# Kernel optimization log

Measured on AMD Instinct MI355X. Metric: run time of the kernel, lower is better.

Reference implementation:

```python
import jax, jax.numpy as jnp
import numpy as np

HEADS = 8
DIM = 512
DIM_HEAD = DIM // 8        # 64
M = DIM // 2               # 256 landmarks
PINV_ITERS = 6
KERNEL = 33                # residual depthwise conv kernel (33,1)


def moore_penrose_pinv(x, iters):
    # x: [b, h, m, m]; Newton-Schulz style iterative pseudoinverse (lucidrains impl)
    abs_x = jnp.abs(x)
    col = abs_x.sum(axis=-1)
    row = abs_x.sum(axis=-2)
    z = jnp.swapaxes(x, -1, -2) / (jnp.max(col) * jnp.max(row))
    I = jnp.eye(x.shape[-1], dtype=x.dtype)
    for _ in range(iters):
        xz = x @ z
        z = 0.25 * z @ (13.0 * I - xz @ (15.0 * I - xz @ (7.0 * I - xz)))
    return z


def setup_inputs() -> dict:
    key = jax.random.key(0)
    ks = jax.random.split(key, 5)
    b, n, dim = 4, 8192, DIM
    x = jax.random.normal(ks[0], (b, n, dim), dtype=jnp.float32)
    # to_qkv: Linear(dim, 3*inner_dim, bias=False); inner_dim = heads*dim_head = dim
    w_qkv = jax.random.normal(ks[1], (dim, 3 * dim), dtype=jnp.float32) / np.sqrt(dim)
    # to_out: Linear(inner_dim, dim) with bias (dropout = identity in eval)
    w_out = jax.random.normal(ks[2], (dim, dim), dtype=jnp.float32) / np.sqrt(dim)
    b_out = jax.random.normal(ks[3], (dim,), dtype=jnp.float32) * 0.01
    # res_conv: Conv2d(heads, heads, (33,1), padding=(16,0), groups=heads, bias=False)
    conv_w = jax.random.normal(ks[4], (HEADS, 1, KERNEL, 1), dtype=jnp.float32) / np.sqrt(KERNEL)
    return {"x": x, "w_qkv": w_qkv, "w_out": w_out, "b_out": b_out, "conv_w": conv_w}


def nystrom_attention(x, w_qkv, w_out, b_out, conv_w):
    b, n, dim = x.shape
    h, d, m = HEADS, DIM_HEAD, M
    # pad front so seq len divisible by num_landmarks (no-op for n=8192, m=256)
    pad = (m - n % m) % m
    xp = jnp.pad(x, ((0, 0), (pad, 0), (0, 0)))
    np_ = n + pad

    qkv = xp @ w_qkv                                   # [b, np, 3*dim]
    q, k, v = jnp.split(qkv, 3, axis=-1)
    to_heads = lambda t: t.reshape(b, np_, h, d).transpose(0, 2, 1, 3)  # [b,h,np,d]
    q, k, v = to_heads(q), to_heads(k), to_heads(v)
    q = q * (d ** -0.5)

    l = np_ // m                                       # tokens per landmark
    pool = lambda t: t.reshape(b, h, m, l, d).mean(axis=3)  # [b,h,m,d]
    q_l, k_l = pool(q), pool(k)

    attn1 = jax.nn.softmax(jnp.einsum('bhnd,bhmd->bhnm', q, k_l), axis=-1)    # [b,h,np,m]
    attn2 = jax.nn.softmax(jnp.einsum('bhid,bhjd->bhij', q_l, k_l), axis=-1)  # [b,h,m,m]
    attn3 = jax.nn.softmax(jnp.einsum('bhmd,bhnd->bhmn', q_l, k), axis=-1)    # [b,h,m,np]

    attn2_inv = moore_penrose_pinv(attn2, PINV_ITERS)
    out = (attn1 @ attn2_inv) @ (attn3 @ v)            # [b,h,np,d]

    # depthwise conv residual over the sequence axis, per head
    res = jax.lax.conv_general_dilated(
        v, conv_w, window_strides=(1, 1),
        padding=((KERNEL // 2, KERNEL // 2), (0, 0)),
        dimension_numbers=('NCHW', 'OIHW', 'NCHW'),
        feature_group_count=h)
    out = out + res

    out = out.transpose(0, 2, 1, 3).reshape(b, np_, dim)
    out = out @ w_out + b_out
    return out[:, -n:]


def reference(x, w_qkv, w_out, b_out, conv_w):
    return x + nystrom_attention(x, w_qkv, w_out, b_out, conv_w)
```

## Files before the change

kernel.cpp:

```cpp
#include <hip/hip_runtime.h>


#define N_SEQ 8192
#define DMODEL 512
#define NHEAD 8
#define DHEAD 64
#define NLAND 256
#define BH 32

typedef unsigned short u16;
typedef __attribute__((ext_vector_type(8))) short bh8;
typedef __attribute__((ext_vector_type(4))) float fx4;

__device__ __forceinline__ float bf2f(u16 u) { return __uint_as_float(((unsigned)u) << 16); }
__device__ __forceinline__ u16 f2bf(float f) {
    unsigned x = __float_as_uint(f);
    return (u16)((x + 0x7fffu + ((x >> 16) & 1u)) >> 16);
}
__device__ __forceinline__ fx4 mfma16(bh8 a, bh8 b, fx4 c) {
    return __builtin_amdgcn_mfma_f32_16x16x32_bf16(a, b, c, 0, 0, 0);
}
__device__ __forceinline__ void gload16(u16* lds, const u16* g) {
    __builtin_amdgcn_global_load_lds(
        (const __attribute__((address_space(1))) unsigned int*)g,
        (__attribute__((address_space(3))) unsigned int*)lds, 16, 0, 0);
}

__global__ void detect_kernel(const u16* __restrict__ X, unsigned* flag_out)
{
    __shared__ int cnt;
    if (threadIdx.x == 0) cnt = 0;
    __syncthreads();
    u16 u = X[threadIdx.x * 2];
    int e = (u >> 7) & 0xFF;
    int insane = (u != 0) && (e < 90 || e > 140);
    atomicAdd(&cnt, insane);
    __syncthreads();
    if (threadIdx.x == 0) flag_out[0] = (cnt > 64) ? 1u : 0u;
}

__global__ __launch_bounds__(256) void convert_kernel(
    const void* __restrict__ in, u16* __restrict__ out, int n, const unsigned* __restrict__ flag)
{
    int i = blockIdx.x * 256 + threadIdx.x;
    if (i >= n) return;
    if (flag[0]) out[i] = f2bf(((const float*)in)[i]);
    else         out[i] = ((const u16*)in)[i];
}

__global__ __launch_bounds__(256) void wtrans_kernel(
    const void* __restrict__ in, u16* __restrict__ out, int rows, int cols,
    const unsigned* __restrict__ flag)
{
    int idx = blockIdx.x * 256 + threadIdx.x;
    if (idx >= rows * cols) return;
    int r = idx / cols, c = idx % cols;
    float v = flag[0] ? ((const float*)in)[idx] : bf2f(((const u16*)in)[idx]);
    out[(size_t)c * rows + r] = f2bf(v);
}

__global__ __launch_bounds__(256) void f2b_kernel(const float* __restrict__ in, u16* __restrict__ out, int n)
{
    int i = blockIdx.x * 256 + threadIdx.x;
    if (i < n) out[i] = f2bf(in[i]);
}

__global__ __launch_bounds__(256) void qkv_mfma_kernel(
    const u16* __restrict__ X, const u16* __restrict__ WT,
    u16* __restrict__ Q, u16* __restrict__ K, u16* __restrict__ VT)
{
    __shared__ u16 Xs[128 * 64];
    __shared__ u16 Ws[128 * 64];
    const int tid = threadIdx.x;
    const int wave = tid >> 6, lane = tid & 63;
    const int wrow = (wave >> 1) * 64, wcol = (wave & 1) * 64;
    const int i0 = blockIdx.x * 128;
    const int j0 = blockIdx.y * 128;
    const int la = lane >> 3, lb = lane & 7;
    const int lm = lane & 15, lq = lane >> 4;
    const int sw = lm & 7;
    const int sc = (lb ^ la) * 8;
    fx4 acc[4][4];
#pragma unroll
    for (int a = 0; a < 4; ++a)
#pragma unroll
        for (int b = 0; b < 4; ++b) acc[a][b] = (fx4){0.f, 0.f, 0.f, 0.f};

    for (int k0 = 0; k0 < DMODEL; k0 += 64) {
        __syncthreads();
#pragma unroll
        for (int jj = 0; jj < 4; ++jj) {
            int rb = wave * 32 + jj * 8;
            gload16(Xs + rb * 64, X + (size_t)(i0 + rb + la) * DMODEL + k0 + sc);
            gload16(Ws + rb * 64, WT + (size_t)(j0 + rb + la) * DMODEL + k0 + sc);
        }
        __syncthreads();
#pragma unroll
        for (int ks = 0; ks < 2; ++ks) {
            const int po = ((ks * 4 + lq) ^ sw) * 8;
            bh8 xf[4], wf[4];
#pragma unroll
            for (int im = 0; im < 4; ++im)
                xf[im] = *(const bh8*)(Xs + (wrow + im * 16 + lm) * 64 + po);
#pragma unroll
            for (int in = 0; in < 4; ++in)
                wf[in] = *(const bh8*)(Ws + (wcol + in * 16 + lm) * 64 + po);
#pragma unroll
            for (int im = 0; im < 4; ++im)
#pragma unroll
                for (int in = 0; in < 4; ++in)
                    acc[im][in] = mfma16(wf[in], xf[im], acc[im][in]);
        }
    }
#pragma unroll
    for (int im = 0; im < 4; ++im) {
        int m = i0 + wrow + im * 16 + lm;
        int bb = m >> 13, ns = m & (N_SEQ - 1);
#pragma unroll
        for (int in = 0; in < 4; ++in) {
            int nn = j0 + wcol + in * 16 + (lq << 2);
            int which = nn >> 9;
            int h = (nn >> 6) & 7;
            int d = nn & 63;
            if (which == 2) {
                size_t vb = (size_t)(bb * NHEAD + h) * DHEAD;
#pragma unroll
                for (int cc = 0; cc < 4; ++cc)
                    VT[(vb + d + cc) * N_SEQ + ns] = f2bf(acc[im][in][cc]);
            } else {
                u16* dst = (which == 0) ? Q : K;
                float s = (which == 0) ? 0.125f : 1.f;
                ushort4 o;
                o.x = f2bf(acc[im][in][0] * s); o.y = f2bf(acc[im][in][1] * s);
                o.z = f2bf(acc[im][in][2] * s); o.w = f2bf(acc[im][in][3] * s);
                *(ushort4*)(dst + ((size_t)(bb * NHEAD + h) * N_SEQ + ns) * DHEAD + d) = o;
            }
        }
    }
}

__global__ __launch_bounds__(64) void pool_kernel(
    const u16* __restrict__ Q, const u16* __restrict__ K,
    float* __restrict__ QL, float* __restrict__ KL,
    u16* __restrict__ QLb, u16* __restrict__ KLb)
{
    int m = blockIdx.x, bh = blockIdx.y, d = threadIdx.x;
    size_t base = ((size_t)bh * N_SEQ + m * 32) * DHEAD + d;
    float sq = 0.f, sk = 0.f;
#pragma unroll
    for (int i = 0; i < 32; ++i) {
        sq += bf2f(Q[base + i * DHEAD]);
        sk += bf2f(K[base + i * DHEAD]);
    }
    size_t ob = ((size_t)bh * NLAND + m) * DHEAD + d;
    sq *= (1.f / 32.f); sk *= (1.f / 32.f);
    QL[ob] = sq; KL[ob] = sk;
    QLb[ob] = f2bf(sq); KLb[ob] = f2bf(sk);
}

__global__ __launch_bounds__(256) void attn2_kernel(
    const float* __restrict__ QL, const float* __restrict__ KL, float* __restrict__ A2)
{
    __shared__ float qrow[64];
    __shared__ float red[256];
    int i = blockIdx.x, bh = blockIdx.y, j = threadIdx.x;
    if (j < 64) qrow[j] = QL[((size_t)bh * NLAND + i) * DHEAD + j];
    __syncthreads();
    const float* kr = KL + ((size_t)bh * NLAND + j) * DHEAD;
    float lg = 0.f;
#pragma unroll
    for (int d = 0; d < 64; ++d) lg += qrow[d] * kr[d];
    red[j] = lg; __syncthreads();
    for (int s = 128; s > 0; s >>= 1) { if (j < s) red[j] = fmaxf(red[j], red[j + s]); __syncthreads(); }
    float mx = red[0]; __syncthreads();
    float p = __expf(lg - mx);
    red[j] = p; __syncthreads();
    for (int s = 128; s > 0; s >>= 1) { if (j < s) red[j] += red[j + s]; __syncthreads(); }
    float sum = red[0];
    A2[((size_t)bh * NLAND + i) * NLAND + j] = p / sum;
}

__global__ void init_scal_kernel(unsigned* scal) { if (threadIdx.x < 2) scal[threadIdx.x] = 0u; }

__global__ __launch_bounds__(256) void absmax_kernel(const float* __restrict__ A2, unsigned* scal)
{
    __shared__ float red[256];
    int bh = blockIdx.x, t = threadIdx.x;
    const float* Ab = A2 + (size_t)bh * 65536;
    float cs = 0.f, rs = 0.f;
    for (int j = 0; j < 256; ++j) cs += fabsf(Ab[t * 256 + j]);
    for (int i = 0; i < 256; ++i) rs += fabsf(Ab[i * 256 + t]);
    red[t] = cs; __syncthreads();
    for (int s = 128; s > 0; s >>= 1) { if (t < s) red[t] = fmaxf(red[t], red[t + s]); __syncthreads(); }
    if (t == 0) atomicMax(scal + 0, __float_as_uint(red[0]));
    __syncthreads();
    red[t] = rs; __syncthreads();
    for (int s = 128; s > 0; s >>= 1) { if (t < s) red[t] = fmaxf(red[t], red[t + s]); __syncthreads(); }
    if (t == 0) atomicMax(scal + 1, __float_as_uint(red[0]));
}

__global__ __launch_bounds__(256) void z0_kernel(
    const float* __restrict__ A2, const unsigned* __restrict__ scal,
    u16* __restrict__ zb, u16* __restrict__ zbT)
{
    float inv = 1.f / (__uint_as_float(scal[0]) * __uint_as_float(scal[1]));
    size_t idx = (size_t)blockIdx.x * 256 + threadIdx.x;
    size_t bh = idx >> 16;
    int r = (int)(idx & 65535);
    int i = r >> 8, j = r & 255;
    zb[idx]  = f2bf(A2[(bh << 16) + (size_t)j * 256 + i] * inv);
    zbT[idx] = f2bf(A2[idx] * inv);
}

__global__ __launch_bounds__(256) void bgemm_mfma_kernel(
    const u16* __restrict__ A, const u16* __restrict__ BT,
    u16* __restrict__ Cn, u16* __restrict__ Ct, const u16* __restrict__ E,
    int N, long sB, long sCn, long sCt, float sc, float alpha, float beta, int wn, int wt)
{
    __shared__ u16 As[64 * 40];
    __shared__ u16 Bs[64 * 40];
    const int tid = threadIdx.x;
    const int wave = tid >> 6, lane = tid & 63;
    const int wm = (wave >> 1) * 32, wnn = (wave & 1) * 32;
    const int i0 = blockIdx.x * 64, j0 = blockIdx.y * 64, bh = blockIdx.z;
    const u16* Ab = A + (size_t)bh * 65536;
    const u16* Bb = BT + (size_t)bh * sB;
    const int lr = tid >> 2, lk = (tid & 3) * 8;
    const int lm = lane & 15, lq = lane >> 4;
    fx4 acc[2][2];
#pragma unroll
    for (int a = 0; a < 2; ++a)
#pragma unroll
        for (int b = 0; b < 2; ++b) acc[a][b] = (fx4){0.f, 0.f, 0.f, 0.f};

    for (int k0 = 0; k0 < 256; k0 += 32) {
        uint4 a4 = *(const uint4*)(Ab + (size_t)(i0 + lr) * 256 + k0 + lk);
        uint4 b4 = *(const uint4*)(Bb + (size_t)(j0 + lr) * 256 + k0 + lk);
        __syncthreads();
        *(uint4*)(As + lr * 40 + lk) = a4;
        *(uint4*)(Bs + lr * 40 + lk) = b4;
        __syncthreads();
        bh8 lf[2], rf[2];
#pragma unroll
        for (int im = 0; im < 2; ++im)
            lf[im] = *(const bh8*)(As + (wm + im * 16 + lm) * 40 + lq * 8);
#pragma unroll
        for (int in = 0; in < 2; ++in)
            rf[in] = *(const bh8*)(Bs + (wnn + in * 16 + lm) * 40 + lq * 8);
#pragma unroll
        for (int im = 0; im < 2; ++im)
#pragma unroll
            for (int in = 0; in < 2; ++in)
                acc[im][in] = mfma16(lf[im], rf[in], acc[im][in]);
    }
#pragma unroll
    for (int im = 0; im < 2; ++im) {
#pragma unroll
        for (int in = 0; in < 2; ++in) {
            int n = j0 + wnn + in * 16 + lm;
            int m0 = i0 + wm + im * 16 + (lq << 2);
            float c[4];
#pragma unroll
            for (int r = 0; r < 4; ++r) {
                int m = m0 + r;
                float x = beta * acc[im][in][r];
                if (alpha != 0.f)
                    x += alpha * bf2f(E[(size_t)bh * 65536 + (size_t)m * 256 + n]);
                if (m == n) x += sc;
                c[r] = x;
            }
            if (wn) {
#pragma unroll
                for (int r = 0; r < 4; ++r)
                    Cn[(size_t)bh * sCn + (size_t)(m0 + r) * N + n] = f2bf(c[r]);
            }
            if (wt) {
                ushort4 o;
                o.x = f2bf(c[0]); o.y = f2bf(c[1]); o.z = f2bf(c[2]); o.w = f2bf(c[3]);
                *(ushort4*)(Ct + (size_t)bh * sCt + (size_t)n * 256 + m0) = o;
            }
        }
    }
}

__global__ __launch_bounds__(256) void attn3v_mfma_kernel(
    const u16* __restrict__ QLb, const u16* __restrict__ Kb,
    const u16* __restrict__ VTb, u16* __restrict__ PO, float* __restrict__ ML)
{
    __shared__ u16 Pl[4][32 * 72];
    const int tid = threadIdx.x;
    const int wave = tid >> 6, lane = tid & 63;
    const int q = lane >> 4, l15 = lane & 15;
    const int m0 = blockIdx.x * 32;
    const int part = blockIdx.y * 4 + wave;
    const int bh = blockIdx.z;
    const int nbase = part * 512;
    u16* Pw = Pl[wave];
    bh8 qf[2][2];
#pragma unroll
    for (int mt = 0; mt < 2; ++mt)
#pragma unroll
        for (int ks = 0; ks < 2; ++ks)
            qf[mt][ks] = *(const bh8*)(QLb + ((size_t)bh * NLAND + m0 + mt * 16 + l15) * DHEAD + ks * 32 + q * 8);
    float M[2] = {-1e30f, -1e30f};
    float L[2] = {0.f, 0.f};
    fx4 O[2][4];
#pragma unroll
    for (int mt = 0; mt < 2; ++mt)
#pragma unroll
        for (int dt = 0; dt < 4; ++dt) O[mt][dt] = (fx4){0.f, 0.f, 0.f, 0.f};

    for (int c = 0; c < 8; ++c) {
        const int n0 = nbase + c * 64;
        fx4 S[4][2];
#pragma unroll
        for (int nt = 0; nt < 4; ++nt)
#pragma unroll
            for (int mt = 0; mt < 2; ++mt) S[nt][mt] = (fx4){0.f, 0.f, 0.f, 0.f};
#pragma unroll
        for (int ks = 0; ks < 2; ++ks)
#pragma unroll
            for (int nt = 0; nt < 4; ++nt) {
                bh8 kf = *(const bh8*)(Kb + ((size_t)bh * N_SEQ + n0 + nt * 16 + l15) * DHEAD + ks * 32 + q * 8);
                S[nt][0] = mfma16(kf, qf[0][ks], S[nt][0]);
                S[nt][1] = mfma16(kf, qf[1][ks], S[nt][1]);
            }
#pragma unroll
        for (int mt = 0; mt < 2; ++mt) {
            float cm = -1e30f;
#pragma unroll
            for (int nt = 0; nt < 4; ++nt)
#pragma unroll
                for (int r = 0; r < 4; ++r) cm = fmaxf(cm, S[nt][mt][r]);
            cm = fmaxf(cm, __shfl_xor(cm, 16));
            cm = fmaxf(cm, __shfl_xor(cm, 32));
            float Mn = fmaxf(M[mt], cm);
            float al = __expf(M[mt] - Mn);
            M[mt] = Mn;
            L[mt] *= al;
#pragma unroll
            for (int dt = 0; dt < 4; ++dt) {
                O[mt][dt][0] *= al; O[mt][dt][1] *= al;
                O[mt][dt][2] *= al; O[mt][dt][3] *= al;
            }
            float ps = 0.f;
#pragma unroll
            for (int nt = 0; nt < 4; ++nt)
#pragma unroll
                for (int r = 0; r < 4; ++r) {
                    float p = __expf(S[nt][mt][r] - Mn);
                    ps += p;
                    Pw[(mt * 16 + l15) * 72 + nt * 16 + q * 4 + r] = f2bf(p);
                }
            ps += __shfl_xor(ps, 16);
            ps += __shfl_xor(ps, 32);
            L[mt] += ps;
        }
#pragma unroll
        for (int ks = 0; ks < 2; ++ks) {
            bh8 pf[2];
#pragma unroll
            for (int mt = 0; mt < 2; ++mt)
                pf[mt] = *(const bh8*)(Pw + (mt * 16 + l15) * 72 + ks * 32 + q * 8);
#pragma unroll
            for (int dt = 0; dt < 4; ++dt) {
                bh8 vf = *(const bh8*)(VTb + ((size_t)bh * DHEAD + dt * 16 + l15) * N_SEQ + n0 + ks * 32 + q * 8);
                O[0][dt] = mfma16(vf, pf[0], O[0][dt]);
                O[1][dt] = mfma16(vf, pf[1], O[1][dt]);
            }
        }
    }
#pragma unroll
    for (int mt = 0; mt < 2; ++mt) {
        size_t mrow = (size_t)(bh * 16 + part) * NLAND + m0 + mt * 16 + l15;
#pragma unroll
        for (int dt = 0; dt < 4; ++dt) {
            ushort4 o;
            o.x = f2bf(O[mt][dt][0]); o.y = f2bf(O[mt][dt][1]);
            o.z = f2bf(O[mt][dt][2]); o.w = f2bf(O[mt][dt][3]);
            *(ushort4*)(PO + mrow * DHEAD + dt * 16 + q * 4) = o;
        }
        if (q == 0) { ML[mrow * 2] = M[mt]; ML[mrow * 2 + 1] = L[mt]; }
    }
}

__global__ __launch_bounds__(64) void combine_kernel(
    const u16* __restrict__ PO, const float* __restrict__ ML, u16* __restrict__ W3VT)
{
    int m = blockIdx.x, bh = blockIdx.y, d = threadIdx.x;
    float Mg = -1e30f;
#pragma unroll
    for (int p = 0; p < 16; ++p)
        Mg = fmaxf(Mg, ML[((size_t)(bh * 16 + p) * NLAND + m) * 2]);
    float denom = 0.f, o = 0.f;
#pragma unroll
    for (int p = 0; p < 16; ++p) {
        size_t ix = (size_t)(bh * 16 + p) * NLAND + m;
        float w = __expf(ML[ix * 2] - Mg);
        denom += ML[ix * 2 + 1] * w;
        o += bf2f(PO[ix * DHEAD + d]) * w;
    }
    W3VT[((size_t)bh * DHEAD + d) * NLAND + m] = f2bf(o / denom);
}

__global__ __launch_bounds__(256) void conv_kernel(
    const u16* __restrict__ VT, const u16* __restrict__ CW, u16* __restrict__ RT)
{
    __shared__ float vl[2080];
    __shared__ float cws[33];
    const int tid = threadIdx.x;
    const int c0 = blockIdx.x * 2048;
    const int row = blockIdx.y;
    const int h = (row >> 6) & 7;
    const u16* src = VT + (size_t)row * N_SEQ;
    for (int i = tid; i < 2080; i += 256) {
        int gn = c0 - 16 + i;
        vl[i] = (gn >= 0 && gn < N_SEQ) ? bf2f(src[gn]) : 0.f;
    }
    if (tid < 33) cws[tid] = bf2f(CW[h * 33 + tid]);
    __syncthreads();
    float v[40];
    const int base = tid * 8;
#pragma unroll
    for (int i = 0; i < 40; ++i) v[i] = vl[base + i];
    float s[8];
#pragma unroll
    for (int j = 0; j < 8; ++j) {
        float a = 0.f;
#pragma unroll
        for (int t = 0; t < 33; ++t) a += cws[t] * v[j + t];
        s[j] = a;
    }
    u16* dst = RT + (size_t)row * N_SEQ + c0 + base;
    ushort4 o0, o1;
    o0.x = f2bf(s[0]); o0.y = f2bf(s[1]); o0.z = f2bf(s[2]); o0.w = f2bf(s[3]);
    o1.x = f2bf(s[4]); o1.y = f2bf(s[5]); o1.z = f2bf(s[6]); o1.w = f2bf(s[7]);
    *(ushort4*)dst = o0;
    *(ushort4*)(dst + 4) = o1;
}

__global__ __launch_bounds__(256) void outheads_mfma_kernel(
    const u16* __restrict__ Qb, const u16* __restrict__ KLb,
    const u16* __restrict__ WMT, const u16* __restrict__ RT,
    u16* __restrict__ Y)
{
    __shared__ u16 Pl[64 * 264];
    __shared__ float wmax[4][64];
    __shared__ float wsum[4][64];
    const int tid = threadIdx.x;
    const int wave = tid >> 6, lane = tid & 63;
    const int q = lane >> 4, l15 = lane & 15;
    const int bh = blockIdx.y;
    const int bb = bh >> 3, h = bh & 7;
    const int n0 = blockIdx.x * 64;
    fx4 S[4][4];
#pragma unroll
    for (int a = 0; a < 4; ++a)
#pragma unroll
        for (int b = 0; b < 4; ++b) S[a][b] = (fx4){0.f, 0.f, 0.f, 0.f};
#pragma unroll
    for (int ks = 0; ks < 2; ++ks) {
        bh8 qfr[4];
#pragma unroll
        for (int nt = 0; nt < 4; ++nt)
            qfr[nt] = *(const bh8*)(Qb + ((size_t)bh * N_SEQ + n0 + nt * 16 + l15) * DHEAD + ks * 32 + q * 8);
#pragma unroll
        for (int mt = 0; mt < 4; ++mt) {
            bh8 kf = *(const bh8*)(KLb + ((size_t)bh * NLAND + wave * 64 + mt * 16 + l15) * DHEAD + ks * 32 + q * 8);
#pragma unroll
            for (int nt = 0; nt < 4; ++nt)
                S[nt][mt] = mfma16(qfr[nt], kf, S[nt][mt]);
        }
    }
#pragma unroll
    for (int nt = 0; nt < 4; ++nt)
#pragma unroll
        for (int r = 0; r < 4; ++r) {
            float pm = fmaxf(fmaxf(S[nt][0][r], S[nt][1][r]), fmaxf(S[nt][2][r], S[nt][3][r]));
            pm = fmaxf(pm, __shfl_xor(pm, 1));
            pm = fmaxf(pm, __shfl_xor(pm, 2));
            pm = fmaxf(pm, __shfl_xor(pm, 4));
            pm = fmaxf(pm, __shfl_xor(pm, 8));
            if (l15 == 0) wmax[wave][nt * 16 + q * 4 + r] = pm;
        }
    __syncthreads();
#pragma unroll
    for (int nt = 0; nt < 4; ++nt)
#pragma unroll
        for (int r = 0; r < 4; ++r) {
            int nl = nt * 16 + q * 4 + r;
            float Mf = fmaxf(fmaxf(wmax[0][nl], wmax[1][nl]), fmaxf(wmax[2][nl], wmax[3][nl]));
            float ps = 0.f;
#pragma unroll
            for (int mt = 0; mt < 4; ++mt) {
                float p = __expf(S[nt][mt][r] - Mf);
                ps += p;
                Pl[nl * 264 + wave * 64 + mt * 16 + l15] = f2bf(p);
            }
            ps += __shfl_xor(ps, 1);
            ps += __shfl_xor(ps, 2);
            ps += __shfl_xor(ps, 4);
            ps += __shfl_xor(ps, 8);
            if (l15 == 0) wsum[wave][nl] = ps;
        }
    __syncthreads();
    fx4 O[4];
#pragma unroll
    for (int nt = 0; nt < 4; ++nt) O[nt] = (fx4){0.f, 0.f, 0.f, 0.f};
#pragma unroll
    for (int ks = 0; ks < 8; ++ks) {
        bh8 af = *(const bh8*)(WMT + ((size_t)bh * DHEAD + wave * 16 + l15) * NLAND + ks * 32 + q * 8);
#pragma unroll
        for (int nt = 0; nt < 4; ++nt) {
            bh8 pf = *(const bh8*)(Pl + (size_t)(nt * 16 + l15) * 264 + ks * 32 + q * 8);
            O[nt] = mfma16(af, pf, O[nt]);
        }
    }
#pragma unroll
    for (int nt = 0; nt < 4; ++nt) {
        int nl = nt * 16 + l15;
        float inv = 1.f / (wsum[0][nl] + wsum[1][nl] + wsum[2][nl] + wsum[3][nl]);
        int d0 = wave * 16 + (q << 2);
        fx4 v = O[nt];
#pragma unroll
        for (int c = 0; c < 4; ++c)
            v[c] = v[c] * inv + bf2f(RT[(size_t)(bh * DHEAD + d0 + c) * N_SEQ + n0 + nl]);
        ushort4 o;
        o.x = f2bf(v[0]); o.y = f2bf(v[1]); o.z = f2bf(v[2]); o.w = f2bf(v[3]);
        *(ushort4*)(Y + ((size_t)bb * N_SEQ + n0 + nl) * DMODEL + h * DHEAD + d0) = o;
    }
}

__global__ __launch_bounds__(256) void final_mfma_kernel(
    const u16* __restrict__ Y, const u16* __restrict__ WT,
    const u16* __restrict__ Bias, const u16* __restrict__ X, void* __restrict__ Out,
    const unsigned* __restrict__ flag)
{
    __shared__ u16 Xs[128 * 64];
    __shared__ u16 Ws[128 * 64];
    const int tid = threadIdx.x;
    const int wave = tid >> 6, lane = tid & 63;
    const int wrow = (wave >> 1) * 64, wcol = (wave & 1) * 64;
    const int i0 = blockIdx.x * 128;
    const int j0 = blockIdx.y * 128;
    const int la = lane >> 3, lb = lane & 7;
    const int lm = lane & 15, lq = lane >> 4;
    const int sw = lm & 7;
    const int sc = (lb ^ la) * 8;
    const unsigned isf32 = flag[0];
    fx4 acc[4][4];
#pragma unroll
    for (int a = 0; a < 4; ++a)
#pragma unroll
        for (int b = 0; b < 4; ++b) acc[a][b] = (fx4){0.f, 0.f, 0.f, 0.f};

    for (int k0 = 0; k0 < DMODEL; k0 += 64) {
        __syncthreads();
#pragma unroll
        for (int jj = 0; jj < 4; ++jj) {
            int rb = wave * 32 + jj * 8;
            gload16(Xs + rb * 64, Y + (size_t)(i0 + rb + la) * DMODEL + k0 + sc);
            gload16(Ws + rb * 64, WT + (size_t)(j0 + rb + la) * DMODEL + k0 + sc);
        }
        __syncthreads();
#pragma unroll
        for (int ks = 0; ks < 2; ++ks) {
            const int po = ((ks * 4 + lq) ^ sw) * 8;
            bh8 xf[4], wf[4];
#pragma unroll
            for (int im = 0; im < 4; ++im)
                xf[im] = *(const bh8*)(Xs + (wrow + im * 16 + lm) * 64 + po);
#pragma unroll
            for (int in = 0; in < 4; ++in)
                wf[in] = *(const bh8*)(Ws + (wcol + in * 16 + lm) * 64 + po);
#pragma unroll
            for (int im = 0; im < 4; ++im)
#pragma unroll
                for (int in = 0; in < 4; ++in)
                    acc[im][in] = mfma16(wf[in], xf[im], acc[im][in]);
        }
    }
#pragma unroll
    for (int im = 0; im < 4; ++im) {
        int m = i0 + wrow + im * 16 + lm;
#pragma unroll
        for (int in = 0; in < 4; ++in) {
            int nn = j0 + wcol + in * 16 + (lq << 2);
            ushort4 b4 = *(const ushort4*)(Bias + nn);
            ushort4 x4 = *(const ushort4*)(X + (size_t)m * DMODEL + nn);
            float c0 = acc[im][in][0] + bf2f(b4.x) + bf2f(x4.x);
            float c1 = acc[im][in][1] + bf2f(b4.y) + bf2f(x4.y);
            float c2 = acc[im][in][2] + bf2f(b4.z) + bf2f(x4.z);
            float c3 = acc[im][in][3] + bf2f(b4.w) + bf2f(x4.w);
            if (isf32) {
                *(float4*)((float*)Out + (size_t)m * DMODEL + nn) = make_float4(c0, c1, c2, c3);
            } else {
                ushort4 o;
                o.x = f2bf(c0); o.y = f2bf(c1); o.z = f2bf(c2); o.w = f2bf(c3);
                *(ushort4*)((u16*)Out + (size_t)m * DMODEL + nn) = o;
            }
        }
    }
}

extern "C" void kernel_launch(void* const* d_in, const int* in_sizes, int n_in,
                              void* d_out, int out_size, void* d_ws, size_t ws_size,
                              hipStream_t stream)
{
    (void)in_sizes; (void)n_in; (void)out_size; (void)ws_size;
    char* ws = (char*)d_ws;
    u16*   Xc    = (u16*)(ws + 0);
    u16*   WqkvT = (u16*)(ws + 33554432);
    u16*   WoutT = (u16*)(ws + 35127296);
    u16*   Boutc = (u16*)(ws + 35651584);
    u16*   CWc   = (u16*)(ws + 35652608);
    u16*   Qb    = (u16*)(ws + 35653632);
    u16*   Kb    = (u16*)(ws + 69208064);
    u16*   RT    = (u16*)(ws + 69208064);
    u16*   VTb   = (u16*)(ws + 102762496);
    float* QL    = (float*)(ws + 136316928);
    float* KL    = (float*)(ws + 138414080);
    u16*   QLb   = (u16*)(ws + 140511232);
    u16*   KLb   = (u16*)(ws + 141559808);
    u16*   W3VT  = (u16*)(ws + 142608384);
    u16*   WMT   = (u16*)(ws + 143656960);
    u16*   A2b   = (u16*)(ws + 144705536);
    u16*   zA    = (u16*)(ws + 148899840);
    u16*   zAT   = (u16*)(ws + 153094144);
    float* A2    = (float*)(ws + 157288448);
    u16*   PO    = (u16*)(ws + 157288448);
    float* ML    = (float*)(ws + 174065664);
    u16*   zB    = (u16*)(ws + 165677056);
    u16*   zBT   = (u16*)(ws + 169871360);
    u16*   xz    = (u16*)(ws + 174065664);
    u16*   xzT   = (u16*)(ws + 178259968);
    u16*   t2T   = (u16*)(ws + 182454272);
    u16*   t3T   = (u16*)(ws + 186648576);
    u16*   Yb    = (u16*)(ws + 157288448);
    unsigned* SCAL = (unsigned*)(ws + 190842880);

    detect_kernel<<<1, 256, 0, stream>>>((const u16*)d_in[0], SCAL + 2);
    convert_kernel<<<65536, 256, 0, stream>>>(d_in[0], Xc, 16777216, SCAL + 2);
    wtrans_kernel<<<3072, 256, 0, stream>>>(d_in[1], WqkvT, 512, 1536, SCAL + 2);
    wtrans_kernel<<<1024, 256, 0, stream>>>(d_in[2], WoutT, 512, 512, SCAL + 2);
    convert_kernel<<<2, 256, 0, stream>>>(d_in[3], Boutc, 512, SCAL + 2);
    convert_kernel<<<2, 256, 0, stream>>>(d_in[4], CWc, 264, SCAL + 2);

    qkv_mfma_kernel<<<dim3(256, 12), 256, 0, stream>>>(Xc, WqkvT, Qb, Kb, VTb);
    pool_kernel<<<dim3(256, BH), 64, 0, stream>>>(Qb, Kb, QL, KL, QLb, KLb);
    attn2_kernel<<<dim3(256, BH), 256, 0, stream>>>(QL, KL, A2);
    init_scal_kernel<<<1, 64, 0, stream>>>(SCAL);
    absmax_kernel<<<32, 256, 0, stream>>>(A2, SCAL);
    z0_kernel<<<8192, 256, 0, stream>>>(A2, SCAL, zA, zAT);
    f2b_kernel<<<8192, 256, 0, stream>>>(A2, A2b, 2097152);

    attn3v_mfma_kernel<<<dim3(8, 4, BH), 256, 0, stream>>>(QLb, Kb, VTb, PO, ML);
    combine_kernel<<<dim3(256, BH), 64, 0, stream>>>(PO, ML, W3VT);
    conv_kernel<<<dim3(4, 2048), 256, 0, stream>>>(VTb, CWc, RT);

    u16 *z = zA, *zT = zAT, *zn = zB, *znT = zBT;
    for (int it = 0; it < 6; ++it) {
        bgemm_mfma_kernel<<<dim3(4, 4, 32), 256, 0, stream>>>(
            A2b, zT, xz, xzT, A2b, 256, 65536, 65536, 65536, 0.f, 0.f, 1.f, 1, 1);
        bgemm_mfma_kernel<<<dim3(4, 4, 32), 256, 0, stream>>>(
            xz, xzT, xz, t2T, xz, 256, 65536, 65536, 65536, 15.f, -7.f, 1.f, 0, 1);
        bgemm_mfma_kernel<<<dim3(4, 4, 32), 256, 0, stream>>>(
            xz, t2T, xz, t3T, xz, 256, 65536, 65536, 65536, 13.f, 0.f, -1.f, 0, 1);
        bgemm_mfma_kernel<<<dim3(4, 4, 32), 256, 0, stream>>>(
            z, t3T, zn, znT, xz, 256, 65536, 65536, 65536, 0.f, 0.f, 0.25f, 1, 1);
        u16* t;
        t = z; z = zn; zn = t;
        t = zT; zT = znT; znT = t;
    }
    bgemm_mfma_kernel<<<dim3(4, 1, 32), 256, 0, stream>>>(
        z, W3VT, WMT, WMT, xz, 64, 16384, 16384, 16384, 0.f, 0.f, 1.f, 0, 1);
    outheads_mfma_kernel<<<dim3(128, BH), 256, 0, stream>>>(Qb, KLb, WMT, RT, Yb);
    final_mfma_kernel<<<dim3(256, 4), 256, 0, stream>>>(Yb, WoutT, Boutc, Xc, d_out, SCAL + 2);
}
```

Before: 809.1 us.

## Stage K/V in LDS for attn3v, widen bgemm k-tile, vectorize convert, fuse f2b

Measured after the change: 720.8 us. 10.9% less time.

```diff
diff --git a/kernel.cpp b/kernel.cpp
--- a/kernel.cpp
+++ b/kernel.cpp
@@ -39,13 +39,19 @@
     if (threadIdx.x == 0) flag_out[0] = (cnt > 64) ? 1u : 0u;
 }
 
-__global__ __launch_bounds__(256) void convert_kernel(
-    const void* __restrict__ in, u16* __restrict__ out, int n, const unsigned* __restrict__ flag)
+__global__ __launch_bounds__(256) void convert4_kernel(
+    const void* __restrict__ in, u16* __restrict__ out, int n4, const unsigned* __restrict__ flag)
 {
     int i = blockIdx.x * 256 + threadIdx.x;
-    if (i >= n) return;
-    if (flag[0]) out[i] = f2bf(((const float*)in)[i]);
-    else         out[i] = ((const u16*)in)[i];
+    if (i >= n4) return;
+    if (flag[0]) {
+        float4 v = ((const float4*)in)[i];
+        ushort4 o;
+        o.x = f2bf(v.x); o.y = f2bf(v.y); o.z = f2bf(v.z); o.w = f2bf(v.w);
+        ((ushort4*)out)[i] = o;
+    } else {
+        ((ushort4*)out)[i] = ((const ushort4*)in)[i];
+    }
 }
 
 __global__ __launch_bounds__(256) void wtrans_kernel(
@@ -57,12 +63,6 @@
     int r = idx / cols, c = idx % cols;
     float v = flag[0] ? ((const float*)in)[idx] : bf2f(((const u16*)in)[idx]);
     out[(size_t)c * rows + r] = f2bf(v);
-}
-
-__global__ __launch_bounds__(256) void f2b_kernel(const float* __restrict__ in, u16* __restrict__ out, int n)
-{
-    int i = blockIdx.x * 256 + threadIdx.x;
-    if (i < n) out[i] = f2bf(in[i]);
 }
 
 __global__ __launch_bounds__(256) void qkv_mfma_kernel(
@@ -201,15 +201,17 @@
 
 __global__ __launch_bounds__(256) void z0_kernel(
     const float* __restrict__ A2, const unsigned* __restrict__ scal,
-    u16* __restrict__ zb, u16* __restrict__ zbT)
+    u16* __restrict__ zb, u16* __restrict__ zbT, u16* __restrict__ A2b)
 {
     float inv = 1.f / (__uint_as_float(scal[0]) * __uint_as_float(scal[1]));
     size_t idx = (size_t)blockIdx.x * 256 + threadIdx.x;
     size_t bh = idx >> 16;
     int r = (int)(idx & 65535);
     int i = r >> 8, j = r & 255;
+    float a = A2[idx];
     zb[idx]  = f2bf(A2[(bh << 16) + (size_t)j * 256 + i] * inv);
-    zbT[idx] = f2bf(A2[idx] * inv);
+    zbT[idx] = f2bf(a * inv);
+    A2b[idx] = f2bf(a);
 }
 
 __global__ __launch_bounds__(256) void bgemm_mfma_kernel(
@@ -217,15 +219,15 @@
     u16* __restrict__ Cn, u16* __restrict__ Ct, const u16* __restrict__ E,
     int N, long sB, long sCn, long sCt, float sc, float alpha, float beta, int wn, int wt)
 {
-    __shared__ u16 As[64 * 40];
-    __shared__ u16 Bs[64 * 40];
+    __shared__ u16 As[64 * 72];
+    __shared__ u16 Bs[64 * 72];
     const int tid = threadIdx.x;
     const int wave = tid >> 6, lane = tid & 63;
     const int wm = (wave >> 1) * 32, wnn = (wave & 1) * 32;
     const int i0 = blockIdx.x * 64, j0 = blockIdx.y * 64, bh = blockIdx.z;
     const u16* Ab = A + (size_t)bh * 65536;
     const u16* Bb = BT + (size_t)bh * sB;
-    const int lr = tid >> 2, lk = (tid & 3) * 8;
+    const int srow = tid >> 2, scol = (tid & 3) * 16;
     const int lm = lane & 15, lq = lane >> 4;
     fx4 acc[2][2];
 #pragma unroll
@@ -233,25 +235,32 @@
 #pragma unroll
         for (int b = 0; b < 2; ++b) acc[a][b] = (fx4){0.f, 0.f, 0.f, 0.f};
 
-    for (int k0 = 0; k0 < 256; k0 += 32) {
-        uint4 a4 = *(const uint4*)(Ab + (size_t)(i0 + lr) * 256 + k0 + lk);
-        uint4 b4 = *(const uint4*)(Bb + (size_t)(j0 + lr) * 256 + k0 + lk);
+    for (int k0 = 0; k0 < 256; k0 += 64) {
+        uint4 a0 = *(const uint4*)(Ab + (size_t)(i0 + srow) * 256 + k0 + scol);
+        uint4 a1 = *(const uint4*)(Ab + (size_t)(i0 + srow) * 256 + k0 + scol + 8);
+        uint4 b0 = *(const uint4*)(Bb + (size_t)(j0 + srow) * 256 + k0 + scol);
+        uint4 b1 = *(const uint4*)(Bb + (size_t)(j0 + srow) * 256 + k0 + scol + 8);
         __syncthreads();
-        *(uint4*)(As + lr * 40 + lk) = a4;
-        *(uint4*)(Bs + lr * 40 + lk) = b4;
+        *(uint4*)(As + srow * 72 + scol) = a0;
+        *(uint4*)(As + srow * 72 + scol + 8) = a1;
+        *(uint4*)(Bs + srow * 72 + scol) = b0;
+        *(uint4*)(Bs + srow * 72 + scol + 8) = b1;
         __syncthreads();
-        bh8 lf[2], rf[2];
-#pragma unroll
-        for (int im = 0; im < 2; ++im)
-            lf[im] = *(const bh8*)(As + (wm + im * 16 + lm) * 40 + lq * 8);
-#pragma unroll
-        for (int in = 0; in < 2; ++in)
-            rf[in] = *(const bh8*)(Bs + (wnn + in * 16 + lm) * 40 + lq * 8);
-#pragma unroll
-        for (int im = 0; im < 2; ++im)
+#pragma unroll
+        for (int ks = 0; ks < 2; ++ks) {
+            bh8 lf[2], rf[2];
+#pragma unroll
+            for (int im = 0; im < 2; ++im)
+                lf[im] = *(const bh8*)(As + (wm + im * 16 + lm) * 72 + ks * 32 + lq * 8);
 #pragma unroll
             for (int in = 0; in < 2; ++in)
-                acc[im][in] = mfma16(lf[im], rf[in], acc[im][in]);
+                rf[in] = *(const bh8*)(Bs + (wnn + in * 16 + lm) * 72 + ks * 32 + lq * 8);
+#pragma unroll
+            for (int im = 0; im < 2; ++im)
+#pragma unroll
+                for (int in = 0; in < 2; ++in)
+                    acc[im][in] = mfma16(lf[im], rf[in], acc[im][in]);
+        }
     }
 #pragma unroll
     for (int im = 0; im < 2; ++im) {
@@ -283,50 +292,66 @@
     }
 }
 
-__global__ __launch_bounds__(256) void attn3v_mfma_kernel(
+__global__ __launch_bounds__(256, 2) void attn3v_mfma_kernel(
     const u16* __restrict__ QLb, const u16* __restrict__ Kb,
     const u16* __restrict__ VTb, u16* __restrict__ PO, float* __restrict__ ML)
 {
-    __shared__ u16 Pl[4][32 * 72];
+    __shared__ u16 Ks[64 * 72];
+    __shared__ u16 Vs[64 * 72];
+    __shared__ u16 Pw[4][64 * 72];
     const int tid = threadIdx.x;
     const int wave = tid >> 6, lane = tid & 63;
     const int q = lane >> 4, l15 = lane & 15;
-    const int m0 = blockIdx.x * 32;
-    const int part = blockIdx.y * 4 + wave;
-    const int bh = blockIdx.z;
+    const int part = blockIdx.x;
+    const int bh = blockIdx.y;
     const int nbase = part * 512;
-    u16* Pw = Pl[wave];
-    bh8 qf[2][2];
-#pragma unroll
-    for (int mt = 0; mt < 2; ++mt)
+    const int srow = tid >> 2, scol = (tid & 3) * 16;
+    u16* Pp = Pw[wave];
+    bh8 qf[4][2];
+#pragma unroll
+    for (int mt = 0; mt < 4; ++mt)
 #pragma unroll
         for (int ks = 0; ks < 2; ++ks)
-            qf[mt][ks] = *(const bh8*)(QLb + ((size_t)bh * NLAND + m0 + mt * 16 + l15) * DHEAD + ks * 32 + q * 8);
-    float M[2] = {-1e30f, -1e30f};
-    float L[2] = {0.f, 0.f};
-    fx4 O[2][4];
-#pragma unroll
-    for (int mt = 0; mt < 2; ++mt)
+            qf[mt][ks] = *(const bh8*)(QLb + ((size_t)bh * NLAND + wave * 64 + mt * 16 + l15) * DHEAD + ks * 32 + q * 8);
+    float M[4] = {-1e30f, -1e30f, -1e30f, -1e30f};
+    float L[4] = {0.f, 0.f, 0.f, 0.f};
+    fx4 O[4][4];
+#pragma unroll
+    for (int mt = 0; mt < 4; ++mt)
 #pragma unroll
         for (int dt = 0; dt < 4; ++dt) O[mt][dt] = (fx4){0.f, 0.f, 0.f, 0.f};
 
     for (int c = 0; c < 8; ++c) {
         const int n0 = nbase + c * 64;
-        fx4 S[4][2];
+        uint4 k0v = *(const uint4*)(Kb + ((size_t)bh * N_SEQ + n0 + srow) * DHEAD + scol);
+        uint4 k1v = *(const uint4*)(Kb + ((size_t)bh * N_SEQ + n0 + srow) * DHEAD + scol + 8);
+        uint4 v0v = *(const uint4*)(VTb + ((size_t)bh * DHEAD + srow) * N_SEQ + n0 + scol);
+        uint4 v1v = *(const uint4*)(VTb + ((size_t)bh * DHEAD + srow) * N_SEQ + n0 + scol + 8);
+        __syncthreads();
+        *(uint4*)(Ks + srow * 72 + scol) = k0v;
+        *(uint4*)(Ks + srow * 72 + scol + 8) = k1v;
+        *(uint4*)(Vs + srow * 72 + scol) = v0v;
+        *(uint4*)(Vs + srow * 72 + scol + 8) = v1v;
+        __syncthreads();
+        fx4 S[4][4];
 #pragma unroll
         for (int nt = 0; nt < 4; ++nt)
 #pragma unroll
-            for (int mt = 0; mt < 2; ++mt) S[nt][mt] = (fx4){0.f, 0.f, 0.f, 0.f};
-#pragma unroll
-        for (int ks = 0; ks < 2; ++ks)
-#pragma unroll
-            for (int nt = 0; nt < 4; ++nt) {
-                bh8 kf = *(const bh8*)(Kb + ((size_t)bh * N_SEQ + n0 + nt * 16 + l15) * DHEAD + ks * 32 + q * 8);
-                S[nt][0] = mfma16(kf, qf[0][ks], S[nt][0]);
-                S[nt][1] = mfma16(kf, qf[1][ks], S[nt][1]);
-            }
-#pragma unroll
-        for (int mt = 0; mt < 2; ++mt) {
+            for (int mt = 0; mt < 4; ++mt) S[nt][mt] = (fx4){0.f, 0.f, 0.f, 0.f};
+#pragma unroll
+        for (int ks = 0; ks < 2; ++ks) {
+            bh8 kf[4];
+#pragma unroll
+            for (int nt = 0; nt < 4; ++nt)
+                kf[nt] = *(const bh8*)(Ks + (nt * 16 + l15) * 72 + ks * 32 + q * 8);
+#pragma unroll
+            for (int nt = 0; nt < 4; ++nt)
+#pragma unroll
+                for (int mt = 0; mt < 4; ++mt)
+                    S[nt][mt] = mfma16(kf[nt], qf[mt][ks], S[nt][mt]);
+        }
+#pragma unroll
+        for (int mt = 0; mt < 4; ++mt) {
             float cm = -1e30f;
 #pragma unroll
             for (int nt = 0; nt < 4; ++nt)
@@ -350,7 +375,7 @@
                 for (int r = 0; r < 4; ++r) {
                     float p = __expf(S[nt][mt][r] - Mn);
                     ps += p;
-                    Pw[(mt * 16 + l15) * 72 + nt * 16 + q * 4 + r] = f2bf(p);
+                    Pp[(mt * 16 + l15) * 72 + nt * 16 + q * 4 + r] = f2bf(p);
                 }
             ps += __shfl_xor(ps, 16);
             ps += __shfl_xor(ps, 32);
@@ -358,21 +383,22 @@
         }
 #pragma unroll
         for (int ks = 0; ks < 2; ++ks) {
-            bh8 pf[2];
-#pragma unroll
-            for (int mt = 0; mt < 2; ++mt)
-                pf[mt] = *(const bh8*)(Pw + (mt * 16 + l15) * 72 + ks * 32 + q * 8);
+            bh8 pf[4];
+#pragma unroll
+            for (int mt = 0; mt < 4; ++mt)
+                pf[mt] = *(const bh8*)(Pp + (mt * 16 + l15) * 72 + ks * 32 + q * 8);
 #pragma unroll
             for (int dt = 0; dt < 4; ++dt) {
-                bh8 vf = *(const bh8*)(VTb + ((size_t)bh * DHEAD + dt * 16 + l15) * N_SEQ + n0 + ks * 32 + q * 8);
-                O[0][dt] = mfma16(vf, pf[0], O[0][dt]);
-                O[1][dt] = mfma16(vf, pf[1], O[1][dt]);
+                bh8 vf = *(const bh8*)(Vs + (dt * 16 + l15) * 72 + ks * 32 + q * 8);
+#pragma unroll
+                for (int mt = 0; mt < 4; ++mt)
+                    O[mt][dt] = mfma16(vf, pf[mt], O[mt][dt]);
             }
         }
     }
 #pragma unroll
-    for (int mt = 0; mt < 2; ++mt) {
-        size_t mrow = (size_t)(bh * 16 + part) * NLAND + m0 + mt * 16 + l15;
+    for (int mt = 0; mt < 4; ++mt) {
+        size_t mrow = (size_t)(bh * 16 + part) * NLAND + wave * 64 + mt * 16 + l15;
 #pragma unroll
         for (int dt = 0; dt < 4; ++dt) {
             ushort4 o;
@@ -640,21 +666,20 @@
     unsigned* SCAL = (unsigned*)(ws + 190842880);
 
     detect_kernel<<<1, 256, 0, stream>>>((const u16*)d_in[0], SCAL + 2);
-    convert_kernel<<<65536, 256, 0, stream>>>(d_in[0], Xc, 16777216, SCAL + 2);
+    convert4_kernel<<<16384, 256, 0, stream>>>(d_in[0], Xc, 4194304, SCAL + 2);
     wtrans_kernel<<<3072, 256, 0, stream>>>(d_in[1], WqkvT, 512, 1536, SCAL + 2);
     wtrans_kernel<<<1024, 256, 0, stream>>>(d_in[2], WoutT, 512, 512, SCAL + 2);
-    convert_kernel<<<2, 256, 0, stream>>>(d_in[3], Boutc, 512, SCAL + 2);
-    convert_kernel<<<2, 256, 0, stream>>>(d_in[4], CWc, 264, SCAL + 2);
+    convert4_kernel<<<1, 256, 0, stream>>>(d_in[3], Boutc, 128, SCAL + 2);
+    convert4_kernel<<<1, 256, 0, stream>>>(d_in[4], CWc, 66, SCAL + 2);
 
     qkv_mfma_kernel<<<dim3(256, 12), 256, 0, stream>>>(Xc, WqkvT, Qb, Kb, VTb);
     pool_kernel<<<dim3(256, BH), 64, 0, stream>>>(Qb, Kb, QL, KL, QLb, KLb);
     attn2_kernel<<<dim3(256, BH), 256, 0, stream>>>(QL, KL, A2);
     init_scal_kernel<<<1, 64, 0, stream>>>(SCAL);
     absmax_kernel<<<32, 256, 0, stream>>>(A2, SCAL);
-    z0_kernel<<<8192, 256, 0, stream>>>(A2, SCAL, zA, zAT);
-    f2b_kernel<<<8192, 256, 0, stream>>>(A2, A2b, 2097152);
-
-    attn3v_mfma_kernel<<<dim3(8, 4, BH), 256, 0, stream>>>(QLb, Kb, VTb, PO, ML);
+    z0_kernel<<<8192, 256, 0, stream>>>(A2, SCAL, zA, zAT, A2b);
+
+    attn3v_mfma_kernel<<<dim3(16, BH), 256, 0, stream>>>(QLb, Kb, VTb, PO, ML);
     combine_kernel<<<dim3(256, BH), 64, 0, stream>>>(PO, ML, W3VT);
     conv_kernel<<<dim3(4, 2048), 256, 0, stream>>>(VTb, CWc, RT);
 
```
